# Performance work log

Hardware: AMD Instinct MI355X
Metric: run time of the kernel (lower is better)

The kernel has to match this reference:

```python
import jax, jax.numpy as jnp
import numpy as np

N = 100000   # nodes
E = 1600000  # edges
D = 256      # emb_dim
H = 512      # 2*emb_dim hidden in GIN MLP
L = 5        # num_layer
NUM_NODE_TYPES = 300
EDGE_FEAT = 7


def setup_inputs() -> dict:
    key = jax.random.key(0)
    ks = jax.random.split(key, 16)
    s = 0.05
    return {
        "x": jax.random.randint(ks[0], (N, 1), 0, NUM_NODE_TYPES, dtype=jnp.int32),
        "edge_index": jax.random.randint(ks[1], (2, E), 0, N, dtype=jnp.int32),
        "edge_attr": jax.random.normal(ks[2], (E, EDGE_FEAT), dtype=jnp.float32),
        "batch": jnp.zeros((N,), dtype=jnp.int32),
        "node_emb": jax.random.normal(ks[3], (NUM_NODE_TYPES, D), dtype=jnp.float32) * s,
        "We": jax.random.normal(ks[4], (L, EDGE_FEAT, D), dtype=jnp.float32) * s,
        "be": jnp.zeros((L, D), dtype=jnp.float32),
        "W1": jax.random.normal(ks[5], (L, D, H), dtype=jnp.float32) * s,
        "b1": jnp.zeros((L, H), dtype=jnp.float32),
        "g1": jnp.ones((L, H), dtype=jnp.float32),
        "bt1": jnp.zeros((L, H), dtype=jnp.float32),
        "W2": jax.random.normal(ks[6], (L, H, D), dtype=jnp.float32) * s,
        "b2": jnp.zeros((L, D), dtype=jnp.float32),
        "eps": jnp.zeros((L,), dtype=jnp.float32),
        "g_bn": jnp.ones((L, D), dtype=jnp.float32),
        "b_bn": jnp.zeros((L, D), dtype=jnp.float32),
    }


def _batchnorm(z, g, b):
    # training-mode BN over the node dim, biased variance, eps=1e-5 (torch default)
    mu = jnp.mean(z, axis=0)
    var = jnp.mean((z - mu) ** 2, axis=0)
    return (z - mu) * jax.lax.rsqrt(var + 1e-5) * g + b


def reference(x, edge_index, edge_attr, batch, node_emb, We, be, W1, b1, g1, bt1,
              W2, b2, eps, g_bn, b_bn):
    src, dst = edge_index[0], edge_index[1]
    h = node_emb[x[:, 0]]                      # [N, D]
    n = h.shape[0]
    for l in range(L):
        edge_emb = edge_attr @ We[l] + be[l]   # [E, D]
        msg = jax.nn.relu(h[src] + edge_emb)   # gather + elementwise message
        agg = jax.ops.segment_sum(msg, dst, num_segments=n)  # scatter-add
        z = (1.0 + eps[l]) * h + agg
        z = jax.nn.relu(_batchnorm(z @ W1[l] + b1[l], g1[l], bt1[l])) @ W2[l] + b2[l]
        z = _batchnorm(z, g_bn[l], b_bn[l])
        h = jax.nn.relu(z) if l != L - 1 else z  # relu on all but last; dropout p=0
    return h  # JK='last'
```

## Files before the change

### kernel.cpp

```cpp
#include <hip/hip_runtime.h>
#include <hip/hip_bf16.h>

#define N_NODES 100000
#define N_EDGES 1600000
#define DIM 256
#define HID 512
#define NLAYERS 5
#define BKP 40
#define MTILES 782

typedef unsigned short u16;
typedef unsigned int u32;
typedef short s16x8 __attribute__((ext_vector_type(8)));
typedef float f32x4 __attribute__((ext_vector_type(4)));

__device__ __forceinline__ float b2f_(u16 u) {
  union { unsigned i; float f; } v;
  v.i = ((unsigned)u) << 16;
  return v.f;
}
__device__ __forceinline__ u16 f2b_(float f) {
  __hip_bfloat16 h = __float2bfloat16(f);
  return *reinterpret_cast<u16*>(&h);
}
__device__ __forceinline__ int pk2_(u16 lo, u16 hi) {
  return (int)(((u32)hi << 16) | (u32)lo);
}
__device__ __forceinline__ void split_pack_(f32x4 a, f32x4 b, int4& hi, int4& lo) {
  float v[8];
  u16 h[8], l[8];
#pragma unroll
  for (int q = 0; q < 4; ++q) { v[q] = a[q]; v[4 + q] = b[q]; }
#pragma unroll
  for (int q = 0; q < 8; ++q) {
    h[q] = f2b_(v[q]);
    l[q] = f2b_(v[q] - b2f_(h[q]));
  }
  hi = make_int4(pk2_(h[0], h[1]), pk2_(h[2], h[3]), pk2_(h[4], h[5]), pk2_(h[6], h[7]));
  lo = make_int4(pk2_(l[0], l[1]), pk2_(l[2], l[3]), pk2_(l[4], l[5]), pk2_(l[6], l[7]));
}
__device__ __forceinline__ int4 bn_pack_(int4 raw, const float* __restrict__ scl,
                                         const float* __restrict__ sft) {
  const u16* rp = (const u16*)&raw;
  u16 o[8];
#pragma unroll
  for (int q = 0; q < 8; ++q) {
    float v = fmaf(b2f_(rp[q]), scl[q], sft[q]);
    o[q] = f2b_(fmaxf(v, 0.f));
  }
  return make_int4(pk2_(o[0], o[1]), pk2_(o[2], o[3]), pk2_(o[4], o[5]), pk2_(o[6], o[7]));
}

__global__ void k_fill(float* out, int n, float val) {
  int i = blockIdx.x * 256 + threadIdx.x;
  if (i < n) out[i] = val;
}

__global__ void k_zero(float* p, int n) {
  int i = blockIdx.x * 256 + threadIdx.x;
  if (i < n) p[i] = 0.f;
}

__global__ void k_zeroi(int* p, int n) {
  int i = blockIdx.x * 256 + threadIdx.x;
  if (i < n) p[i] = 0;
}

__global__ void k_gather(const int* x0, const int* x3, const float* emb, float* h) {
  int idx = blockIdx.x * 256 + threadIdx.x;
  int n = idx >> 8, d = idx & 255;
  int t = x0[n] + x3[n];
  h[idx] = emb[(size_t)t * DIM + d];
}

__global__ void k_hist(const int* __restrict__ dst, int* __restrict__ deg) {
  int e = blockIdx.x * 256 + threadIdx.x;
  if (e < N_EDGES) atomicAdd(&deg[dst[e]], 1);
}

__global__ void k_scan1(const int* __restrict__ deg, int* __restrict__ offs,
                        int* __restrict__ bsum) {
  __shared__ int sm[256];
  int tid = threadIdx.x;
  int i = blockIdx.x * 256 + tid;
  int v = (i < N_NODES) ? deg[i] : 0;
  sm[tid] = v;
  __syncthreads();
  for (int d = 1; d < 256; d <<= 1) {
    int t = (tid >= d) ? sm[tid - d] : 0;
    __syncthreads();
    sm[tid] += t;
    __syncthreads();
  }
  if (i < N_NODES) offs[i] = sm[tid] - v;
  if (tid == 0) bsum[blockIdx.x] = sm[255];
}

__global__ void k_scan2(int* __restrict__ bsum, int nb) {
  __shared__ int sm[512];
  int tid = threadIdx.x;
  int v = (tid < nb) ? bsum[tid] : 0;
  sm[tid] = v;
  __syncthreads();
  for (int d = 1; d < 512; d <<= 1) {
    int t = (tid >= d) ? sm[tid - d] : 0;
    __syncthreads();
    sm[tid] += t;
    __syncthreads();
  }
  if (tid < nb) bsum[tid] = sm[tid] - v;
}

__global__ void k_scan3(int* __restrict__ offs, const int* __restrict__ bsum,
                        int* __restrict__ cur) {
  int i = blockIdx.x * 256 + threadIdx.x;
  if (i < N_NODES) {
    offs[i] += bsum[blockIdx.x];
    cur[i] = 0;
  }
  if (i == 0) offs[N_NODES] = N_EDGES;
}

__global__ void k_fillcsr(const int* __restrict__ dst, const int* __restrict__ srcarr,
                          const int* __restrict__ offs, int* __restrict__ cur,
                          int2* __restrict__ elist) {
  int e = blockIdx.x * 256 + threadIdx.x;
  if (e < N_EDGES) {
    int d = dst[e];
    int p = offs[d] + atomicAdd(&cur[d], 1);
    elist[p] = make_int2(srcarr[e], e);
  }
}

template <int BNIN>
__global__ __launch_bounds__(256) void k_agg(
    const float* __restrict__ hin, const float* __restrict__ ea,
    const int2* __restrict__ csr, const int* __restrict__ offs,
    const float* __restrict__ We, const float* __restrict__ be,
    const float* __restrict__ eps_l, const float* __restrict__ scl2,
    const float* __restrict__ sft2, float* __restrict__ z) {
  const int lane = threadIdx.x & 63;
  const int n = blockIdx.x * 4 + (threadIdx.x >> 6);
  const int c0 = lane * 4;
  float w[7][4];
#pragma unroll
  for (int k = 0; k < 7; ++k) {
    f32x4 t = *(const f32x4*)&We[k * DIM + c0];
    w[k][0] = t[0]; w[k][1] = t[1]; w[k][2] = t[2]; w[k][3] = t[3];
  }
  const f32x4 bev = *(const f32x4*)&be[c0];
  f32x4 sv, fv;
  if (BNIN) { sv = *(const f32x4*)&scl2[c0]; fv = *(const f32x4*)&sft2[c0]; }
  const f32x4 hn = *(const f32x4*)&hin[(size_t)n * DIM + c0];
  const float e1p = 1.0f + eps_l[0];
  float acc[4];
#pragma unroll
  for (int q = 0; q < 4; ++q) {
    float hv = hn[q];
    if (BNIN) hv = fmaxf(fmaf(hv, sv[q], fv[q]), 0.f);
    acc[q] = e1p * hv;
  }
  const int eb = offs[n], ee = offs[n + 1];
  int e = eb;
  for (; e + 2 <= ee; e += 2) {
    const int2 sA = csr[e];
    const int2 sB = csr[e + 1];
    const f32x4 hA = *(const f32x4*)&hin[(size_t)sA.x * DIM + c0];
    const f32x4 hB = *(const f32x4*)&hin[(size_t)sB.x * DIM + c0];
    const float* pA = ea + (size_t)sA.y * 7;
    const float* pB = ea + (size_t)sB.y * 7;
    float aA[7], aB[7];
#pragma unroll
    for (int k = 0; k < 7; ++k) { aA[k] = pA[k]; aB[k] = pB[k]; }
#pragma unroll
    for (int q = 0; q < 4; ++q) {
      float hv = hA[q];
      if (BNIN) hv = fmaxf(fmaf(hv, sv[q], fv[q]), 0.f);
      float t = bev[q];
#pragma unroll
      for (int k = 0; k < 7; ++k) t = fmaf(aA[k], w[k][q], t);
      acc[q] += fmaxf(hv + t, 0.f);
    }
#pragma unroll
    for (int q = 0; q < 4; ++q) {
      float hv = hB[q];
      if (BNIN) hv = fmaxf(fmaf(hv, sv[q], fv[q]), 0.f);
      float t = bev[q];
#pragma unroll
      for (int k = 0; k < 7; ++k) t = fmaf(aB[k], w[k][q], t);
      acc[q] += fmaxf(hv + t, 0.f);
    }
  }
  if (e < ee) {
    const int2 sA = csr[e];
    const f32x4 hA = *(const f32x4*)&hin[(size_t)sA.x * DIM + c0];
    const float* pA = ea + (size_t)sA.y * 7;
    float aA[7];
#pragma unroll
    for (int k = 0; k < 7; ++k) aA[k] = pA[k];
#pragma unroll
    for (int q = 0; q < 4; ++q) {
      float hv = hA[q];
      if (BNIN) hv = fmaxf(fmaf(hv, sv[q], fv[q]), 0.f);
      float t = bev[q];
#pragma unroll
      for (int k = 0; k < 7; ++k) t = fmaf(aA[k], w[k][q], t);
      acc[q] += fmaxf(hv + t, 0.f);
    }
  }
  f32x4 o;
#pragma unroll
  for (int q = 0; q < 4; ++q) o[q] = acc[q];
  *(f32x4*)&z[(size_t)n * DIM + c0] = o;
}

template <int K, int NC>
__global__ void k_wconv(const float* __restrict__ W, u16* __restrict__ Wth,
                        u16* __restrict__ Wtl) {
  int idx = blockIdx.x * 256 + threadIdx.x;
  int n = idx / K, k = idx - n * K;
  float w = W[(size_t)k * NC + n];
  u16 hh = f2b_(w);
  Wth[idx] = hh;
  Wtl[idx] = f2b_(w - b2f_(hh));
}

__global__ void k_bnprep(const float* __restrict__ sum, const float* __restrict__ sq,
                         const float* __restrict__ g, const float* __restrict__ bt,
                         float* __restrict__ scl, float* __restrict__ sft, int n) {
  int j = blockIdx.x * 256 + threadIdx.x;
  if (j < n) {
    const float invN = 1.0f / 100000.0f;
    float mu = sum[j] * invN;
    float var = fmaf(-mu, mu, sq[j] * invN);
    float s = g[j] * rsqrtf(var + 1e-5f);
    scl[j] = s;
    sft[j] = fmaf(-mu, s, bt[j]);
  }
}

template <int K, int NC, int NA, int OBF, int BN1A>
__global__ __launch_bounds__(256) void k_mgemm(
    const void* __restrict__ Av, const u16* __restrict__ Bth,
    const u16* __restrict__ Btl, const float* __restrict__ bias,
    void* __restrict__ Ov, float* __restrict__ colsum, float* __restrict__ colsq,
    const float* __restrict__ ascl, const float* __restrict__ asft) {
  __shared__ u16 As[NA * 128 * BKP];
  __shared__ u16 Bs[2 * 128 * BKP];
  const int tid = threadIdx.x;
  const int m0 = blockIdx.x * 128;
  const int n0 = blockIdx.y * 128;
  const int lane = tid & 63;
  const int wv = tid >> 6;
  const int wr = (wv >> 1) * 64;
  const int wc = (wv & 1) * 64;
  const int lr = lane & 15;
  const int kc = (lane >> 4) * 8;
  const int sr = tid >> 1;
  const int sc = (tid & 1) * 16;
  const int ga = min(m0 + sr, N_NODES - 1);
  const int gb = n0 + sr;

  const f32x4 z4 = {0.f, 0.f, 0.f, 0.f};
  f32x4 acc[4][4];
#pragma unroll
  for (int i = 0; i < 4; ++i)
#pragma unroll
    for (int j = 0; j < 4; ++j) acc[i][j] = z4;

  for (int k0 = 0; k0 < K; k0 += 32) {
    int4 a0, a1, al0, al1;
    if (NA == 2) {
      const float* src = (const float*)Av + (size_t)ga * K + k0 + sc;
      f32x4 v0 = *(const f32x4*)(src);
      f32x4 v1 = *(const f32x4*)(src + 4);
      f32x4 v2 = *(const f32x4*)(src + 8);
      f32x4 v3 = *(const f32x4*)(src + 12);
      split_pack_(v0, v1, a0, al0);
      split_pack_(v2, v3, a1, al1);
    } else {
      const u16* src = (const u16*)Av + (size_t)ga * K + k0 + sc;
      a0 = *(const int4*)(src);
      a1 = *(const int4*)(src + 8);
      if (BN1A) {
        a0 = bn_pack_(a0, ascl + k0 + sc, asft + k0 + sc);
        a1 = bn_pack_(a1, ascl + k0 + sc + 8, asft + k0 + sc + 8);
      }
    }
    const u16* bhp = Bth + (size_t)gb * K + k0 + sc;
    const u16* blp = Btl + (size_t)gb * K + k0 + sc;
    int4 b0 = *(const int4*)(bhp);
    int4 b1 = *(const int4*)(bhp + 8);
    int4 b2 = *(const int4*)(blp);
    int4 b3 = *(const int4*)(blp + 8);

    __syncthreads();
    *(int4*)&As[sr * BKP + sc] = a0;
    *(int4*)&As[sr * BKP + sc + 8] = a1;
    if (NA == 2) {
      *(int4*)&As[128 * BKP + sr * BKP + sc] = al0;
      *(int4*)&As[128 * BKP + sr * BKP + sc + 8] = al1;
    }
    *(int4*)&Bs[sr * BKP + sc] = b0;
    *(int4*)&Bs[sr * BKP + sc + 8] = b1;
    *(int4*)&Bs[128 * BKP + sr * BKP + sc] = b2;
    *(int4*)&Bs[128 * BKP + sr * BKP + sc + 8] = b3;
    __syncthreads();

    s16x8 aF[NA][4], bF[2][4];
#pragma unroll
    for (int i = 0; i < 4; ++i) {
      aF[0][i] = *reinterpret_cast<const s16x8*>(&As[(wr + i * 16 + lr) * BKP + kc]);
      if (NA == 2)
        aF[1][i] =
            *reinterpret_cast<const s16x8*>(&As[128 * BKP + (wr + i * 16 + lr) * BKP + kc]);
      bF[0][i] = *reinterpret_cast<const s16x8*>(&Bs[(wc + i * 16 + lr) * BKP + kc]);
      bF[1][i] = *reinterpret_cast<const s16x8*>(&Bs[128 * BKP + (wc + i * 16 + lr) * BKP + kc]);
    }
#pragma unroll
    for (int i = 0; i < 4; ++i)
#pragma unroll
      for (int j = 0; j < 4; ++j) {
        acc[i][j] =
            __builtin_amdgcn_mfma_f32_16x16x32_bf16(aF[0][i], bF[0][j], acc[i][j], 0, 0, 0);
        acc[i][j] =
            __builtin_amdgcn_mfma_f32_16x16x32_bf16(aF[0][i], bF[1][j], acc[i][j], 0, 0, 0);
        if (NA == 2)
          acc[i][j] =
              __builtin_amdgcn_mfma_f32_16x16x32_bf16(aF[1][i], bF[0][j], acc[i][j], 0, 0, 0);
      }
  }

  float bj[4];
#pragma unroll
  for (int j = 0; j < 4; ++j) bj[j] = bias[n0 + wc + j * 16 + lr];
  float ls[4] = {0.f, 0.f, 0.f, 0.f}, lq[4] = {0.f, 0.f, 0.f, 0.f};
#pragma unroll
  for (int i = 0; i < 4; ++i) {
    const int row0 = m0 + wr + i * 16 + (lane >> 4) * 4;
#pragma unroll
    for (int r = 0; r < 4; ++r) {
      const int grow = row0 + r;
      if (grow < N_NODES) {
        const size_t o = (size_t)grow * NC + n0 + wc + lr;
#pragma unroll
        for (int j = 0; j < 4; ++j) {
          float v = acc[i][j][r] + bj[j];
          ls[j] += v;
          lq[j] = fmaf(v, v, lq[j]);
          if (OBF) ((u16*)Ov)[o + j * 16] = f2b_(v);
          else ((float*)Ov)[o + j * 16] = v;
        }
      }
    }
  }
#pragma unroll
  for (int j = 0; j < 4; ++j) {
    float s = ls[j], q = lq[j];
    s += __shfl_xor(s, 16); q += __shfl_xor(q, 16);
    s += __shfl_xor(s, 32); q += __shfl_xor(q, 32);
    if ((lane >> 4) == 0) {
      unsafeAtomicAdd(&colsum[n0 + wc + j * 16 + lr], s);
      unsafeAtomicAdd(&colsq[n0 + wc + j * 16 + lr], q);
    }
  }
}

__global__ void k_bn(const void* Y, int y_bf, const float* sum, const float* sq,
                     const float* g, const float* b, int NC_mask,
                     void* O, int o_bf, int do_relu) {
  int idx = blockIdx.x * 256 + threadIdx.x;
  int j = idx & NC_mask;
  const float invN = 1.0f / 100000.0f;
  float mu = sum[j] * invN;
  float var = fmaf(-mu, mu, sq[j] * invN);
  float v = y_bf ? b2f_(((const u16*)Y)[idx]) : ((const float*)Y)[idx];
  v = fmaf((v - mu) * rsqrtf(var + 1e-5f), g[j], b[j]);
  if (do_relu) v = fmaxf(v, 0.f);
  if (o_bf) ((u16*)O)[idx] = f2b_(v);
  else ((float*)O)[idx] = v;
}

extern "C" void kernel_launch(void* const* d_in, const int* in_sizes, int n_in,
                              void* d_out, int out_size, void* d_ws, size_t ws_size,
                              hipStream_t stream) {
  float* out = (float*)d_out;

  const int expected[16] = {100000, 3200000, 11200000, 100000, 76800, 8960, 1280,
                            655360, 2560, 2560, 2560, 655360, 1280, 5, 1280, 1280};
  float sentinel = 0.f;
  if (n_in != 16) sentinel = 60.f;
  else
    for (int i = 0; i < 16; ++i)
      if (in_sizes[i] != expected[i]) { sentinel = 100.f + (float)i; break; }
  if (sentinel == 0.f && out_size != N_NODES * DIM) sentinel = 90.f;

  const size_t ND = (size_t)N_NODES * DIM;
  const size_t NH = (size_t)N_NODES * HID;
  const size_t base = 4096 * sizeof(float);
  const size_t need_base = base + 2 * ND * sizeof(float) + NH * sizeof(u16);
  if (sentinel == 0.f && ws_size < need_base) sentinel = 77.f;
  if (sentinel != 0.f) {
    k_fill<<<(out_size + 255) / 256, 256, 0, stream>>>(out, out_size, sentinel);
    return;
  }

  float* stats = (float*)d_ws;
  float* sum1 = stats;
  float* sq1 = sum1 + HID;
  float* sum2 = sq1 + HID;
  float* sq2 = sum2 + DIM;
  float* scl1 = stats + 1536;
  float* sft1 = scl1 + HID;
  float* scl2 = sft1 + HID;
  float* sft2 = scl2 + DIM;
  float* bufA = stats + 4096;
  float* bufB = bufA + ND;
  u16* Y1 = (u16*)(bufB + ND);

  const size_t csr_ints = (size_t)N_NODES + (size_t)(N_NODES + 1) + 512 + 1 +
                          2 * (size_t)N_EDGES;
  const int csr_tail = ws_size >= need_base + csr_ints * sizeof(int);
  int* degc = csr_tail ? (int*)((char*)d_ws + need_base) : (int*)Y1;
  int* offs = degc + N_NODES;
  int* bsum = offs + N_NODES + 1;
  int2* elist = (int2*)(bsum + 512 + 1);
  const int NB_N = (N_NODES + 255) / 256;
  const int NB_E = N_EDGES / 256;

  const int* x0 = (const int*)d_in[0];
  const int* ei = (const int*)d_in[1];
  const float* ea = (const float*)d_in[2];
  const int* x3 = (const int*)d_in[3];
  const float* emb = (const float*)d_in[4];
  const float* We = (const float*)d_in[5];
  const float* be = (const float*)d_in[6];
  const float* W1 = (const float*)d_in[7];
  const float* b1 = (const float*)d_in[8];
  const float* g1 = (const float*)d_in[9];
  const float* bt1 = (const float*)d_in[10];
  const float* W2 = (const float*)d_in[11];
  const float* b2 = (const float*)d_in[12];
  const float* eps = (const float*)d_in[13];
  const float* g_bn = (const float*)d_in[14];
  const float* b_bn = (const float*)d_in[15];

  const int* srcs = ei;
  const int* dsts = ei + N_EDGES;

  const int gridND = (int)(ND / 256);

  auto build_csr = [&]() {
    k_zeroi<<<NB_N, 256, 0, stream>>>(degc, N_NODES);
    k_hist<<<NB_E, 256, 0, stream>>>(dsts, degc);
    k_scan1<<<NB_N, 256, 0, stream>>>(degc, offs, bsum);
    k_scan2<<<1, 512, 0, stream>>>(bsum, NB_N);
    k_scan3<<<NB_N, 256, 0, stream>>>(offs, bsum, degc);
    k_fillcsr<<<NB_E, 256, 0, stream>>>(dsts, srcs, offs, degc, elist);
  };

  k_gather<<<gridND, 256, 0, stream>>>(x0, x3, emb, bufA);
  if (csr_tail) build_csr();

  float* bufs[2] = {bufA, bufB};
  int p = 0;
  for (int l = 0; l < NLAYERS; ++l) {
    float* IN = bufs[p];
    float* ZB = bufs[1 - p];
    u16* Wth = (u16*)IN;
    u16* Wtl = Wth + (size_t)DIM * HID;

    if (!csr_tail) build_csr();
    k_zero<<<6, 256, 0, stream>>>(stats, 1536);

    if (l == 0)
      k_agg<0><<<N_NODES / 4, 256, 0, stream>>>(IN, ea, elist, offs,
                                                We + (size_t)l * 7 * DIM,
                                                be + (size_t)l * DIM, eps + l,
                                                nullptr, nullptr, ZB);
    else
      k_agg<1><<<N_NODES / 4, 256, 0, stream>>>(IN, ea, elist, offs,
                                                We + (size_t)l * 7 * DIM,
                                                be + (size_t)l * DIM, eps + l,
                                                scl2, sft2, ZB);

    k_wconv<DIM, HID><<<(DIM * HID) / 256, 256, 0, stream>>>(
        W1 + (size_t)l * DIM * HID, Wth, Wtl);
    k_mgemm<DIM, HID, 2, 1, 0><<<dim3(MTILES, HID / 128), 256, 0, stream>>>(
        ZB, Wth, Wtl, b1 + (size_t)l * HID, Y1, sum1, sq1, nullptr, nullptr);
    k_bnprep<<<2, 256, 0, stream>>>(sum1, sq1, g1 + (size_t)l * HID,
                                    bt1 + (size_t)l * HID, scl1, sft1, HID);

    k_wconv<HID, DIM><<<(DIM * HID) / 256, 256, 0, stream>>>(
        W2 + (size_t)l * HID * DIM, Wth, Wtl);
    k_mgemm<HID, DIM, 1, 0, 1><<<dim3(MTILES, DIM / 128), 256, 0, stream>>>(
        Y1, Wth, Wtl, b2 + (size_t)l * DIM, ZB, sum2, sq2, scl1, sft1);

    if (l != NLAYERS - 1)
      k_bnprep<<<1, 256, 0, stream>>>(sum2, sq2, g_bn + (size_t)l * DIM,
                                      b_bn + (size_t)l * DIM, scl2, sft2, DIM);
    else
      k_bn<<<gridND, 256, 0, stream>>>(ZB, 0, sum2, sq2, g_bn + (size_t)l * DIM,
                                       b_bn + (size_t)l * DIM, DIM - 1, out, 0, 0);
    p ^= 1;
  }
}
```

Before: 3.340 ms.

## Permute edge attributes into CSR order and batch source indices via wave shuffles

The CSR fill now copies each edge's 7 attributes into a destination-sorted array, so the aggregation kernel reads edge features contiguously instead of gathering them by original edge id. The edge list shrinks to source indices only. Each wave loads up to 64 source indices at once and broadcasts them with shuffles, then processes four edges per iteration to keep more gathers in flight. This adds a one-time permuted copy of the edge attributes and more workspace, and if the workspace is too small the CSR (including the copy) is rebuilt every layer.

```diff
diff --git a/kernel.cpp b/kernel.cpp
--- a/kernel.cpp
+++ b/kernel.cpp
@@ -122,20 +122,25 @@
 }
 
 __global__ void k_fillcsr(const int* __restrict__ dst, const int* __restrict__ srcarr,
-                          const int* __restrict__ offs, int* __restrict__ cur,
-                          int2* __restrict__ elist) {
+                          const float* __restrict__ ea, const int* __restrict__ offs,
+                          int* __restrict__ cur, int* __restrict__ elist,
+                          float* __restrict__ eaperm) {
   int e = blockIdx.x * 256 + threadIdx.x;
   if (e < N_EDGES) {
     int d = dst[e];
     int p = offs[d] + atomicAdd(&cur[d], 1);
-    elist[p] = make_int2(srcarr[e], e);
+    elist[p] = srcarr[e];
+    const float* s = ea + (size_t)e * 7;
+    float* o = eaperm + (size_t)p * 7;
+#pragma unroll
+    for (int k = 0; k < 7; ++k) o[k] = s[k];
   }
 }
 
 template <int BNIN>
 __global__ __launch_bounds__(256) void k_agg(
-    const float* __restrict__ hin, const float* __restrict__ ea,
-    const int2* __restrict__ csr, const int* __restrict__ offs,
+    const float* __restrict__ hin, const float* __restrict__ eap,
+    const int* __restrict__ csr, const int* __restrict__ offs,
     const float* __restrict__ We, const float* __restrict__ be,
     const float* __restrict__ eps_l, const float* __restrict__ scl2,
     const float* __restrict__ sft2, float* __restrict__ z) {
@@ -160,52 +165,52 @@
     if (BNIN) hv = fmaxf(fmaf(hv, sv[q], fv[q]), 0.f);
     acc[q] = e1p * hv;
   }
-  const int eb = offs[n], ee = offs[n + 1];
-  int e = eb;
-  for (; e + 2 <= ee; e += 2) {
-    const int2 sA = csr[e];
-    const int2 sB = csr[e + 1];
-    const f32x4 hA = *(const f32x4*)&hin[(size_t)sA.x * DIM + c0];
-    const f32x4 hB = *(const f32x4*)&hin[(size_t)sB.x * DIM + c0];
-    const float* pA = ea + (size_t)sA.y * 7;
-    const float* pB = ea + (size_t)sB.y * 7;
-    float aA[7], aB[7];
-#pragma unroll
-    for (int k = 0; k < 7; ++k) { aA[k] = pA[k]; aB[k] = pB[k]; }
+
+  auto msg = [&](const f32x4& hs, const float* a) {
 #pragma unroll
     for (int q = 0; q < 4; ++q) {
-      float hv = hA[q];
+      float hv = hs[q];
       if (BNIN) hv = fmaxf(fmaf(hv, sv[q], fv[q]), 0.f);
       float t = bev[q];
 #pragma unroll
-      for (int k = 0; k < 7; ++k) t = fmaf(aA[k], w[k][q], t);
+      for (int k = 0; k < 7; ++k) t = fmaf(a[k], w[k][q], t);
       acc[q] += fmaxf(hv + t, 0.f);
     }
-#pragma unroll
-    for (int q = 0; q < 4; ++q) {
-      float hv = hB[q];
-      if (BNIN) hv = fmaxf(fmaf(hv, sv[q], fv[q]), 0.f);
-      float t = bev[q];
-#pragma unroll
-      for (int k = 0; k < 7; ++k) t = fmaf(aB[k], w[k][q], t);
-      acc[q] += fmaxf(hv + t, 0.f);
-    }
-  }
-  if (e < ee) {
-    const int2 sA = csr[e];
-    const f32x4 hA = *(const f32x4*)&hin[(size_t)sA.x * DIM + c0];
-    const float* pA = ea + (size_t)sA.y * 7;
-    float aA[7];
-#pragma unroll
-    for (int k = 0; k < 7; ++k) aA[k] = pA[k];
-#pragma unroll
-    for (int q = 0; q < 4; ++q) {
-      float hv = hA[q];
-      if (BNIN) hv = fmaxf(fmaf(hv, sv[q], fv[q]), 0.f);
-      float t = bev[q];
-#pragma unroll
-      for (int k = 0; k < 7; ++k) t = fmaf(aA[k], w[k][q], t);
-      acc[q] += fmaxf(hv + t, 0.f);
+  };
+
+  const int eb = offs[n], ee = offs[n + 1];
+  for (int base = eb; base < ee; base += 64) {
+    const int m = min(64, ee - base);
+    const int cs = csr[base + min(lane, m - 1)];
+    int e = 0;
+    for (; e + 4 <= m; e += 4) {
+      const int s0 = __shfl(cs, e);
+      const int s1 = __shfl(cs, e + 1);
+      const int s2 = __shfl(cs, e + 2);
+      const int s3 = __shfl(cs, e + 3);
+      const f32x4 h0 = *(const f32x4*)&hin[(size_t)s0 * DIM + c0];
+      const f32x4 h1 = *(const f32x4*)&hin[(size_t)s1 * DIM + c0];
+      const f32x4 h2 = *(const f32x4*)&hin[(size_t)s2 * DIM + c0];
+      const f32x4 h3 = *(const f32x4*)&hin[(size_t)s3 * DIM + c0];
+      const float* p0 = eap + (size_t)(base + e) * 7;
+      float a0[7], a1[7], a2[7], a3[7];
+#pragma unroll
+      for (int k = 0; k < 7; ++k) {
+        a0[k] = p0[k]; a1[k] = p0[7 + k]; a2[k] = p0[14 + k]; a3[k] = p0[21 + k];
+      }
+      msg(h0, a0);
+      msg(h1, a1);
+      msg(h2, a2);
+      msg(h3, a3);
+    }
+    for (; e < m; ++e) {
+      const int s0 = __shfl(cs, e);
+      const f32x4 h0 = *(const f32x4*)&hin[(size_t)s0 * DIM + c0];
+      const float* p0 = eap + (size_t)(base + e) * 7;
+      float a0[7];
+#pragma unroll
+      for (int k = 0; k < 7; ++k) a0[k] = p0[k];
+      msg(h0, a0);
     }
   }
   f32x4 o;
@@ -418,13 +423,15 @@
   float* bufB = bufA + ND;
   u16* Y1 = (u16*)(bufB + ND);
 
-  const size_t csr_ints = (size_t)N_NODES + (size_t)(N_NODES + 1) + 512 + 1 +
-                          2 * (size_t)N_EDGES;
-  const int csr_tail = ws_size >= need_base + csr_ints * sizeof(int);
+  const size_t csr_ints =
+      (size_t)N_NODES + (size_t)(N_NODES + 1) + 512 + 1 + (size_t)N_EDGES;
+  const size_t csr_bytes = csr_ints * sizeof(int) + (size_t)N_EDGES * 7 * sizeof(float);
+  const int csr_tail = ws_size >= need_base + csr_bytes;
   int* degc = csr_tail ? (int*)((char*)d_ws + need_base) : (int*)Y1;
   int* offs = degc + N_NODES;
   int* bsum = offs + N_NODES + 1;
-  int2* elist = (int2*)(bsum + 512 + 1);
+  int* elist = bsum + 512 + 1;
+  float* eaperm = (float*)(elist + N_EDGES);
   const int NB_N = (N_NODES + 255) / 256;
   const int NB_E = N_EDGES / 256;
 
@@ -456,7 +463,7 @@
     k_scan1<<<NB_N, 256, 0, stream>>>(degc, offs, bsum);
     k_scan2<<<1, 512, 0, stream>>>(bsum, NB_N);
     k_scan3<<<NB_N, 256, 0, stream>>>(offs, bsum, degc);
-    k_fillcsr<<<NB_E, 256, 0, stream>>>(dsts, srcs, offs, degc, elist);
+    k_fillcsr<<<NB_E, 256, 0, stream>>>(dsts, srcs, ea, offs, degc, elist, eaperm);
   };
 
   k_gather<<<gridND, 256, 0, stream>>>(x0, x3, emb, bufA);
@@ -474,12 +481,12 @@
     k_zero<<<6, 256, 0, stream>>>(stats, 1536);
 
     if (l == 0)
-      k_agg<0><<<N_NODES / 4, 256, 0, stream>>>(IN, ea, elist, offs,
+      k_agg<0><<<N_NODES / 4, 256, 0, stream>>>(IN, eaperm, elist, offs,
                                                 We + (size_t)l * 7 * DIM,
                                                 be + (size_t)l * DIM, eps + l,
                                                 nullptr, nullptr, ZB);
     else
-      k_agg<1><<<N_NODES / 4, 256, 0, stream>>>(IN, ea, elist, offs,
+      k_agg<1><<<N_NODES / 4, 256, 0, stream>>>(IN, eaperm, elist, offs,
                                                 We + (size_t)l * 7 * DIM,
                                                 be + (size_t)l * DIM, eps + l,
                                                 scl2, sft2, ZB);
```

New measurement: 3.248 ms. -2.8%, faster.
